# Performance work log

Measured on AMD Instinct MI355X. Metric: run time of the kernel, lower is better.

The kernel has to match this reference:

```python
import jax, jax.numpy as jnp
import numpy as np

B, T, N, H = 128, 512, 256, 1024  # batch, seq_len(input_size), num_nodes(params.input_size), hidden_size


def _glorot(k, shape):
    fan_in, fan_out = shape
    s = float(np.sqrt(6.0 / (fan_in + fan_out)))
    return jax.random.uniform(k, shape, minval=-s, maxval=s, dtype=jnp.float32)


def setup_inputs() -> dict:
    key = jax.random.key(0)
    ks = jax.random.split(key, 10)
    return {
        "x": jax.random.normal(ks[0], (B, T, N), dtype=jnp.float32),
        # SAGEConv 1: lin_l (neighbor mean, with bias), lin_r (root, no bias)
        "Wl1": _glorot(ks[1], (T, H)), "Wr1": _glorot(ks[2], (T, H)), "b1": jnp.zeros((H,), jnp.float32),
        # SAGEConv 2
        "Wl2": _glorot(ks[3], (H, H)), "Wr2": _glorot(ks[4], (H, H)), "b2": jnp.zeros((H,), jnp.float32),
        # block_1: Linear(H,H,bias=False), Linear(H,T,bias=False), Sigmoid
        "W1a": _glorot(ks[5], (H, H)), "W1b": _glorot(ks[6], (H, T)),
        # block_2: Linear(N,N,bias=False), Linear(N,H,bias=False), Sigmoid
        "W2a": _glorot(ks[7], (N, N)), "W2b": _glorot(ks[8], (N, H)),
    }


def _sage(h, Wl, Wr, b):
    # Dense graph without self-loops: mean over neighbors = (sum_all - self) / (n-1).
    n = h.shape[1]
    mean_nb = (jnp.sum(h, axis=1, keepdims=True) - h) / (n - 1)  # [B,N,F]
    return mean_nb @ Wl + h @ Wr + b  # SAGEConv: lin_l(aggr) + lin_r(x)


def reference(x, Wl1, Wr1, b1, Wl2, Wr2, b2, W1a, W1b, W2a, W2b):
    h = jnp.transpose(x, (0, 2, 1))            # [B,N,T] nodes=features
    h = _sage(h, Wl1, Wr1, b1)                 # [B,N,H]
    h = _sage(h, Wl2, Wr2, b2)                 # [B,N,H]
    h = jax.nn.sigmoid((h @ W1a) @ W1b)        # [B,N,T]
    h = jnp.transpose(h, (0, 2, 1))            # [B,T,N]
    return jax.nn.sigmoid((h @ W2a) @ W2b)     # [B,T,H]
```

## Files before the change

kernel.cpp:

```cpp
#include <hip/hip_runtime.h>
#include <hip/hip_bf16.h>

#define B_ 128
#define T_ 512
#define N_ 256
#define H_ 1024

typedef unsigned short u16;
typedef __attribute__((ext_vector_type(8))) __bf16 bf16x8;
typedef __attribute__((ext_vector_type(4))) float f32x4;

__device__ __forceinline__ u16 f2bf(float f) {
    unsigned u = __float_as_uint(f);
    u = (u + 0x7FFFu + ((u >> 16) & 1u)) >> 16;
    return (u16)u;
}

__device__ __forceinline__ void g2l16(const void* g, void* l) {
    __builtin_amdgcn_global_load_lds(
        (const __attribute__((address_space(1))) void*)g,
        (__attribute__((address_space(3))) void*)l,
        16, 0, 0);
}

#define ASLOT 12288u

#define GATE(N) { asm volatile("s_waitcnt vmcnt(" #N ")" ::: "memory"); \
                  __builtin_amdgcn_s_barrier(); }
#define LD4(dst, base) { _Pragma("unroll") for (int i_ = 0; i_ < 4; ++i_) \
    dst[i_] = *(const bf16x8*)(L + (base) + i_ * 512); }
#define STAGE(tile) { const u16* a_ = gA + (size_t)(tile) * 32; \
    const u16* b_ = gB + (size_t)(tile) * 32; \
    const unsigned s_ = (unsigned)(((tile) % 3) * ASLOT); \
    g2l16(a_, dA0 + s_);  g2l16(a_ + jstr, dA0 + s_ + 4096); \
    g2l16(b_, dB0 + s_); }
#define BODY(t) { \
    const unsigned sl = (unsigned)(((t) % 3) * ASLOT); \
    bf16x8 ra[4], rb[4]; \
    LD4(ra, sl + aoff); \
    LD4(rb, sl + boff); \
    if ((t) + 2 < nt) STAGE((t) + 2); \
    __builtin_amdgcn_s_setprio(1); \
    _Pragma("unroll") for (int mi_ = 0; mi_ < 4; ++mi_) \
    _Pragma("unroll") for (int ni_ = 0; ni_ < 4; ++ni_) \
        acc[mi_][ni_] = __builtin_amdgcn_mfma_f32_16x16x32_bf16( \
            ra[mi_], rb[ni_], acc[mi_][ni_], 0, 0, 0); \
    __builtin_amdgcn_s_setprio(0); }

template<int ACT, int OUT>
__global__ __launch_bounds__(512, 2) void gemm_e3(
    const u16* __restrict__ A, const u16* __restrict__ Bt,
    float* __restrict__ Cf, u16* __restrict__ Cb,
    const float* __restrict__ bias,
    int Nc, int K, int bshift, int gysh)
{
    __shared__ u16 L[36864];
    const int tid = threadIdx.x;
    const int wave = tid >> 6, lane = tid & 63;
    const int l16 = lane & 15, lh = lane >> 4;
    const int wm = wave >> 1, wn = wave & 1;

    const int qq = (int)gridDim.x >> 3;
    const int orig = (int)blockIdx.x;
    const int wg = (orig & 7) * qq + (orig >> 3);
    const int by = wg & ((1 << gysh) - 1), bx = wg >> gysh;
    const size_t m0 = (size_t)bx * 256, n0 = (size_t)by * 128;

    const int sx8 = (lh ^ ((l16 >> 1) & 3)) * 8;
    const unsigned aoff = (unsigned)(wm * 2048 + l16 * 32 + sx8);
    const unsigned boff = (unsigned)(8192 + wn * 2048 + l16 * 32 + sx8);

    const int srow = tid >> 2;
    const int sslot = (tid & 3) ^ ((srow >> 1) & 3);
    const size_t jstr = (size_t)128 * K;
    const u16* gA = A + (m0 + srow) * (size_t)K + sslot * 8;
    const u16* gB = Bt + (n0 + srow) * (size_t)K + sslot * 8;
    u16* const dA0 = L + (unsigned)(wave * 512);
    u16* const dB0 = L + 8192 + (unsigned)(wave * 512);

    f32x4 acc[4][4] = {};
    const int nt = K >> 5;

    STAGE(0); STAGE(1);
    for (int t = 0; t < nt - 1; ++t) {
        GATE(3);
        BODY(t);
    }
    GATE(0);
    { const int t = nt - 1; BODY(t); }

    const size_t NcS = (size_t)Nc;
    if (OUT == 2) {
        __syncthreads();
        const int P = 260;
#pragma unroll
        for (int mi = 0; mi < 4; ++mi) {
#pragma unroll
            for (int ni = 0; ni < 4; ++ni) {
                int tt = wn * 64 + ni * 16 + l16;
                int nn = wm * 64 + mi * 16 + lh * 4;
                u16 e[4];
#pragma unroll
                for (int rr = 0; rr < 4; ++rr) {
                    float v = acc[mi][ni][rr];
                    v = 1.0f / (1.0f + __expf(-v));
                    e[rr] = f2bf(v);
                }
                *(uint2*)&L[tt * P + nn] = *(const uint2*)e;
            }
        }
        __syncthreads();
        const int t = tid >> 2, seg = tid & 3;
        const u16* src = &L[t * P + seg * 64];
        uint2 u2[16];
#pragma unroll
        for (int j = 0; j < 16; ++j) u2[j] = *(const uint2*)&src[j * 4];
        const size_t b = m0 >> 8;
        u16* dst = Cb + ((b * T_ + (n0 + (size_t)t)) * N_ + seg * 64);
#pragma unroll
        for (int i = 0; i < 8; ++i) {
            uint4 w = make_uint4(u2[2 * i].x, u2[2 * i].y, u2[2 * i + 1].x, u2[2 * i + 1].y);
            ((uint4*)dst)[i] = w;
        }
    } else {
#pragma unroll
        for (int mi = 0; mi < 4; ++mi) {
#pragma unroll
            for (int ni = 0; ni < 4; ++ni) {
                size_t rbase = m0 + wm * 64 + mi * 16 + lh * 4;
                size_t col   = n0 + wn * 64 + ni * 16 + l16;
#pragma unroll
                for (int rr = 0; rr < 4; ++rr) {
                    size_t row = rbase + rr;
                    float v = acc[mi][ni][rr];
                    if (bias) v += bias[(row >> bshift) * NcS + col];
                    if (ACT) v = 1.0f / (1.0f + __expf(-v));
                    if (OUT == 1) __builtin_nontemporal_store(v, &Cf[row * NcS + col]);
                    else          Cb[row * NcS + col] = f2bf(v);
                }
            }
        }
    }
}

__device__ __forceinline__ void small_body(
    const u16* __restrict__ A, const u16* __restrict__ Bt,
    float* __restrict__ Cf, u16* __restrict__ Cb,
    const float* __restrict__ bias,
    int Nc, int K, int lda, int ldb, int outmode, int bshift,
    float kscale, float bmul, int bx, int by)
{
    __shared__ u16 lA[128 * 64];
    __shared__ u16 lB[128 * 64];
    const int tid = threadIdx.x;
    const int wave = tid >> 6, lane = tid & 63;
    const int l16 = lane & 15, lh = lane >> 4;
    const int wm = wave >> 1, wn = wave & 1;
    const long m0 = (long)bx * 128;
    const long n0 = (long)by * 128;

    f32x4 acc[4][4] = {};

    for (int k0 = 0; k0 < K; k0 += 64) {
#pragma unroll
        for (int j = 0; j < 4; ++j) {
            int c = j * 256 + tid;
            int row = c >> 3, col = (c & 7) << 3;
            g2l16(A  + (m0 + row) * (size_t)lda + k0 + col, &lA[(size_t)(j * 256 + (wave << 6)) * 8]);
            g2l16(Bt + (n0 + row) * (size_t)ldb + k0 + col, &lB[(size_t)(j * 256 + (wave << 6)) * 8]);
        }
        __syncthreads();
#pragma unroll
        for (int s = 0; s < 2; ++s) {
            bf16x8 af[4], bfr[4];
#pragma unroll
            for (int mi = 0; mi < 4; ++mi)
                af[mi] = *(const bf16x8*)&lA[((wm << 6) + (mi << 4) + l16) * 64 + s * 32 + (lh << 3)];
#pragma unroll
            for (int ni = 0; ni < 4; ++ni)
                bfr[ni] = *(const bf16x8*)&lB[((wn << 6) + (ni << 4) + l16) * 64 + s * 32 + (lh << 3)];
#pragma unroll
            for (int mi = 0; mi < 4; ++mi)
#pragma unroll
                for (int ni = 0; ni < 4; ++ni)
                    acc[mi][ni] = __builtin_amdgcn_mfma_f32_16x16x32_bf16(af[mi], bfr[ni], acc[mi][ni], 0, 0, 0);
        }
        __syncthreads();
    }

#pragma unroll
    for (int mi = 0; mi < 4; ++mi) {
#pragma unroll
        for (int ni = 0; ni < 4; ++ni) {
            long rbase = m0 + (wm << 6) + (mi << 4) + (lh << 2);
            long col   = n0 + (wn << 6) + (ni << 4) + l16;
#pragma unroll
            for (int r = 0; r < 4; ++r) {
                long row = rbase + r;
                float v = acc[mi][ni][r] * kscale;
                if (outmode == 2) {
                    v += (col < 1024 ? 1.0f : 256.0f / 255.0f) * bias[col & 1023];
                    Cb[(size_t)row * Nc + col] = f2bf(v);
                } else if (outmode == 3) {
                    if (bias) v += bmul * bias[(size_t)(row >> bshift) * Nc + col];
                    atomicAdd(&Cf[(size_t)row * Nc + col], v);
                } else {
                    if (bias) v += bmul * bias[(size_t)(row >> bshift) * Nc + col];
                    if (outmode == 1) Cf[(size_t)row * Nc + col] = v;
                    else              Cb[(size_t)row * Nc + col] = f2bf(v);
                }
            }
        }
    }
}

__global__ __launch_bounds__(256) void gemm_s23(
    const u16* __restrict__ Acat, const u16* __restrict__ W2cat,
    float* __restrict__ t12, const float* __restrict__ b2)
{
    small_body(Acat + blockIdx.x * 256, W2cat + blockIdx.x * 256, t12, nullptr,
               blockIdx.x == 0 ? b2 : nullptr,
               1024, 256, 2048, 2048, 3, 31, 1.0f, 1.0f, 0, blockIdx.y);
}

__global__ __launch_bounds__(256) void k_small4(
    const u16* __restrict__ W2cat, const u16* __restrict__ W1rm, u16* __restrict__ W12t,
    const u16* __restrict__ W1bt, const u16* __restrict__ W1ab, u16* __restrict__ W1ct,
    const u16* __restrict__ W2bt, const u16* __restrict__ W2ab, u16* __restrict__ W2ct,
    const u16* __restrict__ s1b, const u16* __restrict__ Wcat, u16* __restrict__ Acat,
    const float* __restrict__ b1)
{
    const int bid = blockIdx.x;
    if (bid < 32) {
        small_body(W2cat, W1rm, nullptr, W12t, nullptr, 512, 1024, 2048, 1024,
                   0, 0, 1.0f, 0.0f, bid >> 2, bid & 3);
    } else if (bid < 64) {
        int r = bid - 32;
        small_body(W1bt, W1ab, nullptr, W1ct, nullptr, 1024, 1024, 1024, 1024,
                   0, 0, 1.0f, 0.0f, r >> 3, r & 7);
    } else if (bid < 80) {
        int r = bid - 64;
        small_body(W2bt, W2ab, nullptr, W2ct, nullptr, 256, 256, 256, 256,
                   0, 0, 1.0f, 0.0f, r >> 1, r & 1);
    } else {
        int r = bid - 80;
        small_body(s1b, Wcat, nullptr, Acat, b1, 2048, 512, 512, 512,
                   2, 0, 1.0f / 255.0f, 0.0f, 0, r);
    }
}

__global__ __launch_bounds__(256) void k_prep(
    const float* __restrict__ Wl1, const float* __restrict__ Wr1,
    const float* __restrict__ Wl2, const float* __restrict__ Wr2,
    const float* __restrict__ W1b, const float* __restrict__ W2b,
    const float* __restrict__ W1a, const float* __restrict__ W2a,
    u16* __restrict__ Wcat, u16* __restrict__ W1rm,
    u16* __restrict__ W2cat,
    u16* __restrict__ W1bt, u16* __restrict__ W2bt,
    u16* __restrict__ W1ab, u16* __restrict__ W2ab,
    const float* __restrict__ x, u16* __restrict__ h, u16* __restrict__ s1b)
{
    __shared__ float smem[32 * 257];
    int bid = blockIdx.x;
    const int tx = threadIdx.x, ty = threadIdx.y;
    if (bid < 512) {
        float (*tl)[33] = (float(*)[33])smem;
        float (*tr)[33] = (float(*)[33])(smem + 32 * 33);
        int r0 = (bid >> 5) * 32, c0 = (bid & 31) * 32;
#pragma unroll
        for (int i = 0; i < 4; ++i) {
            int r = r0 + ty + 8 * i;
            float wl = Wl1[(size_t)r * H_ + c0 + tx];
            float wr = Wr1[(size_t)r * H_ + c0 + tx];
            tl[ty + 8 * i][tx] = wl;
            tr[ty + 8 * i][tx] = wl + wr;
            W1rm[(size_t)r * H_ + c0 + tx] = f2bf(wr - wl * (1.0f / 255.0f));
        }
        __syncthreads();
#pragma unroll
        for (int i = 0; i < 4; ++i) {
            size_t o = (size_t)(c0 + ty + 8 * i) * T_ + r0 + tx;
            Wcat[o]                     = f2bf(tl[tx][ty + 8 * i]);
            Wcat[o + (size_t)1024 * T_] = f2bf(tr[tx][ty + 8 * i]);
        }
    } else if (bid < 1536) {
        float (*tl)[33] = (float(*)[33])smem;
        float (*tr)[33] = (float(*)[33])(smem + 32 * 33);
        bid -= 512;
        int r0 = (bid >> 5) * 32, c0 = (bid & 31) * 32;
#pragma unroll
        for (int i = 0; i < 4; ++i) {
            int r = r0 + ty + 8 * i;
            float wl = Wl2[(size_t)r * H_ + c0 + tx];
            float wr = Wr2[(size_t)r * H_ + c0 + tx];
            tl[ty + 8 * i][tx] = wr - wl * (1.0f / 255.0f);
            tr[ty + 8 * i][tx] = wl;
        }
        __syncthreads();
#pragma unroll
        for (int i = 0; i < 4; ++i) {
            size_t o = (size_t)(c0 + ty + 8 * i) * 2048 + r0 + tx;
            W2cat[o]        = f2bf(tl[tx][ty + 8 * i]);
            W2cat[o + 1024] = f2bf(tr[tx][ty + 8 * i]);
        }
    } else if (bid < 2048) {
        float (*tl)[33] = (float(*)[33])smem;
        bid -= 1536;
        int r0 = (bid >> 4) * 32, c0 = (bid & 15) * 32;
#pragma unroll
        for (int i = 0; i < 4; ++i)
            tl[ty + 8 * i][tx] = W1b[(size_t)(r0 + ty + 8 * i) * T_ + c0 + tx];
        __syncthreads();
#pragma unroll
        for (int i = 0; i < 4; ++i)
            W1bt[(size_t)(c0 + ty + 8 * i) * H_ + r0 + tx] = f2bf(tl[tx][ty + 8 * i]);
    } else if (bid < 2304) {
        float (*tl)[33] = (float(*)[33])smem;
        bid -= 2048;
        int r0 = (bid >> 5) * 32, c0 = (bid & 31) * 32;
#pragma unroll
        for (int i = 0; i < 4; ++i)
            tl[ty + 8 * i][tx] = W2b[(size_t)(r0 + ty + 8 * i) * H_ + c0 + tx];
        __syncthreads();
#pragma unroll
        for (int i = 0; i < 4; ++i)
            W2bt[(size_t)(c0 + ty + 8 * i) * N_ + r0 + tx] = f2bf(tl[tx][ty + 8 * i]);
    } else if (bid < 2848) {
        int i = (bid - 2304) * 256 + ty * 32 + tx;
        const int n1 = H_ * H_ / 8;
        const float* s; u16* d;
        if (i < n1) { s = W1a; d = W1ab; }
        else        { s = W2a; d = W2ab; i -= n1; }
        float4 a = ((const float4*)s)[2 * i], b = ((const float4*)s)[2 * i + 1];
        u16 e[8] = {f2bf(a.x), f2bf(a.y), f2bf(a.z), f2bf(a.w),
                    f2bf(b.x), f2bf(b.y), f2bf(b.z), f2bf(b.w)};
        ((uint4*)d)[i] = *(const uint4*)e;
    } else {
        float (*sm)[257] = (float(*)[257])smem;
        int bid2 = bid - 2848;
        const int b = bid2 >> 4, t0 = (bid2 & 15) * 32;
        const int tid = ty * 32 + tx;
        const int wave = tid >> 6, lane = tid & 63;
        const float* xb = x + ((size_t)b * T_ + t0) * N_;
#pragma unroll
        for (int i = 0; i < 8; ++i) {
            int j = wave * 8 + i;
            float4 v = *(const float4*)(xb + (size_t)j * N_ + lane * 4);
            sm[j][lane * 4 + 0] = v.x;
            sm[j][lane * 4 + 1] = v.y;
            sm[j][lane * 4 + 2] = v.z;
            sm[j][lane * 4 + 3] = v.w;
        }
        __syncthreads();
#pragma unroll
        for (int i = 0; i < 8; ++i) {
            int j = wave * 8 + i;
            float s = sm[j][lane] + sm[j][lane + 64] + sm[j][lane + 128] + sm[j][lane + 192];
#pragma unroll
            for (int o = 32; o; o >>= 1) s += __shfl_down(s, o, 64);
            if (lane == 0) s1b[(size_t)b * T_ + t0 + j] = f2bf(s);
        }
        u16 e[32];
#pragma unroll
        for (int j = 0; j < 32; ++j) e[j] = f2bf(sm[j][tid]);
        uint4* dst = (uint4*)(h + ((size_t)b * N_ + tid) * T_ + t0);
        const uint4* src = (const uint4*)e;
#pragma unroll
        for (int v = 0; v < 4; ++v) dst[v] = src[v];
    }
}

extern "C" void kernel_launch(void* const* d_in, const int* in_sizes, int n_in,
                              void* d_out, int out_size, void* d_ws, size_t ws_size,
                              hipStream_t stream)
{
    const float* x   = (const float*)d_in[0];
    const float* Wl1 = (const float*)d_in[1];
    const float* Wr1 = (const float*)d_in[2];
    const float* b1  = (const float*)d_in[3];
    const float* Wl2 = (const float*)d_in[4];
    const float* Wr2 = (const float*)d_in[5];
    const float* b2  = (const float*)d_in[6];
    const float* W1a = (const float*)d_in[7];
    const float* W1b = (const float*)d_in[8];
    const float* W2a = (const float*)d_in[9];
    const float* W2b = (const float*)d_in[10];
    float* out = (float*)d_out;

    char* ws = (char*)d_ws;
    size_t off = 0;
    auto alloc = [&](size_t bytes) -> char* {
        char* p = ws + off;
        off += (bytes + 255) & ~(size_t)255;
        return p;
    };

    const size_t BN = (size_t)B_ * N_;
    const size_t BT = (size_t)B_ * T_;

    u16* h_bf   = (u16*)alloc(BN * T_ * 2);
    u16* h2_bf  = (u16*)alloc(BN * H_ * 2);
    u16* Wcat   = (u16*)alloc((size_t)2048 * T_ * 2);
    u16* W1rm   = (u16*)alloc((size_t)T_ * H_ * 2);
    u16* W2cat  = (u16*)alloc((size_t)H_ * 2048 * 2);
    u16* W1bt   = (u16*)alloc((size_t)T_ * H_ * 2);
    u16* W1ab   = (u16*)alloc((size_t)H_ * H_ * 2);
    u16* W1ct   = (u16*)alloc((size_t)T_ * H_ * 2);
    u16* W2bt   = (u16*)alloc((size_t)H_ * N_ * 2);
    u16* W2ab   = (u16*)alloc((size_t)N_ * N_ * 2);
    u16* W2ct   = (u16*)alloc((size_t)H_ * N_ * 2);
    u16* W12t   = (u16*)alloc((size_t)H_ * T_ * 2);
    u16* s1b    = (u16*)alloc(BT * 2);
    u16* Acat   = (u16*)alloc((size_t)B_ * 2048 * 2);
    float* t12  = (float*)alloc((size_t)B_ * H_ * 4);

    u16* q_bf = h_bf;

    hipMemsetAsync(t12, 0, (size_t)B_ * H_ * 4, stream);
    k_prep<<<dim3(4896), dim3(32, 8), 0, stream>>>(Wl1, Wr1, Wl2, Wr2, W1b, W2b, W1a, W2a,
                                                   Wcat, W1rm, W2cat, W1bt, W2bt, W1ab, W2ab,
                                                   x, h_bf, s1b);
    k_small4<<<dim3(96), 256, 0, stream>>>(W2cat, W1rm, W12t, W1bt, W1ab, W1ct,
                                           W2bt, W2ab, W2ct, s1b, Wcat, Acat, b1);
    gemm_s23<<<dim3(8, 8), 256, 0, stream>>>(Acat, W2cat, t12, b2);

    gemm_e3<0, 0><<<dim3(1024), 512, 0, stream>>>(h_bf, W12t, nullptr, h2_bf, t12, H_, T_, 8, 3);
    gemm_e3<1, 2><<<dim3(512), 512, 0, stream>>>(h2_bf, W1ct, nullptr, q_bf, nullptr, T_, H_, 0, 2);
    gemm_e3<1, 1><<<dim3(2048), 512, 0, stream>>>(q_bf, W2ct, out, nullptr, nullptr, H_, N_, 0, 3);
}
```

Baseline: 271.0 us.

## Shrink GEMM tiles to 128x128 with 256-thread blocks and double buffering

Replaces the 256x128 tile, 512-thread, triple-buffered GEMM kernel with a 128x128 tile, 256-thread kernel using double-buffered LDS and a single wait per k-step. This cuts LDS use and raises the number of resident blocks and the grid size, aiming for better occupancy and load balance across CUs. In exchange each tile reuses less data, and the prefetch depth drops from two tiles to one, so more global load latency may be exposed. The transposed sigmoid epilogue is reworked to stage through LDS in two halves to fit the smaller buffer.

```diff
diff --git a/kernel.cpp b/kernel.cpp
--- a/kernel.cpp
+++ b/kernel.cpp
@@ -23,7 +23,7 @@
         16, 0, 0);
 }
 
-#define ASLOT 12288u
+#define ASLOT 8192u
 
 #define GATE(N) { asm volatile("s_waitcnt vmcnt(" #N ")" ::: "memory"); \
                   __builtin_amdgcn_s_barrier(); }
@@ -31,30 +31,18 @@
     dst[i_] = *(const bf16x8*)(L + (base) + i_ * 512); }
 #define STAGE(tile) { const u16* a_ = gA + (size_t)(tile) * 32; \
     const u16* b_ = gB + (size_t)(tile) * 32; \
-    const unsigned s_ = (unsigned)(((tile) % 3) * ASLOT); \
-    g2l16(a_, dA0 + s_);  g2l16(a_ + jstr, dA0 + s_ + 4096); \
-    g2l16(b_, dB0 + s_); }
-#define BODY(t) { \
-    const unsigned sl = (unsigned)(((t) % 3) * ASLOT); \
-    bf16x8 ra[4], rb[4]; \
-    LD4(ra, sl + aoff); \
-    LD4(rb, sl + boff); \
-    if ((t) + 2 < nt) STAGE((t) + 2); \
-    __builtin_amdgcn_s_setprio(1); \
-    _Pragma("unroll") for (int mi_ = 0; mi_ < 4; ++mi_) \
-    _Pragma("unroll") for (int ni_ = 0; ni_ < 4; ++ni_) \
-        acc[mi_][ni_] = __builtin_amdgcn_mfma_f32_16x16x32_bf16( \
-            ra[mi_], rb[ni_], acc[mi_][ni_], 0, 0, 0); \
-    __builtin_amdgcn_s_setprio(0); }
+    const unsigned s_ = (unsigned)(((tile) & 1) * ASLOT); \
+    g2l16(a_, dA0 + s_);  g2l16(a_ + rstr, dA0 + s_ + 2048); \
+    g2l16(b_, dB0 + s_);  g2l16(b_ + rstr, dB0 + s_ + 2048); }
 
 template<int ACT, int OUT>
-__global__ __launch_bounds__(512, 2) void gemm_e3(
+__global__ __launch_bounds__(256, 4) void gemm_e4(
     const u16* __restrict__ A, const u16* __restrict__ Bt,
     float* __restrict__ Cf, u16* __restrict__ Cb,
     const float* __restrict__ bias,
     int Nc, int K, int bshift, int gysh)
 {
-    __shared__ u16 L[36864];
+    __shared__ u16 L[16384];
     const int tid = threadIdx.x;
     const int wave = tid >> 6, lane = tid & 63;
     const int l16 = lane & 15, lh = lane >> 4;
@@ -64,63 +52,75 @@
     const int orig = (int)blockIdx.x;
     const int wg = (orig & 7) * qq + (orig >> 3);
     const int by = wg & ((1 << gysh) - 1), bx = wg >> gysh;
-    const size_t m0 = (size_t)bx * 256, n0 = (size_t)by * 128;
+    const size_t m0 = (size_t)bx * 128, n0 = (size_t)by * 128;
 
     const int sx8 = (lh ^ ((l16 >> 1) & 3)) * 8;
     const unsigned aoff = (unsigned)(wm * 2048 + l16 * 32 + sx8);
-    const unsigned boff = (unsigned)(8192 + wn * 2048 + l16 * 32 + sx8);
+    const unsigned boff = (unsigned)(4096 + wn * 2048 + l16 * 32 + sx8);
 
     const int srow = tid >> 2;
     const int sslot = (tid & 3) ^ ((srow >> 1) & 3);
-    const size_t jstr = (size_t)128 * K;
+    const size_t rstr = (size_t)64 * K;
     const u16* gA = A + (m0 + srow) * (size_t)K + sslot * 8;
     const u16* gB = Bt + (n0 + srow) * (size_t)K + sslot * 8;
     u16* const dA0 = L + (unsigned)(wave * 512);
-    u16* const dB0 = L + 8192 + (unsigned)(wave * 512);
+    u16* const dB0 = L + 4096 + (unsigned)(wave * 512);
 
     f32x4 acc[4][4] = {};
     const int nt = K >> 5;
 
-    STAGE(0); STAGE(1);
-    for (int t = 0; t < nt - 1; ++t) {
-        GATE(3);
-        BODY(t);
-    }
-    GATE(0);
-    { const int t = nt - 1; BODY(t); }
+    STAGE(0);
+    for (int t = 0; t < nt; ++t) {
+        GATE(0);
+        const unsigned sl = (unsigned)((t & 1) * ASLOT);
+        bf16x8 ra[4], rb[4];
+        LD4(ra, sl + aoff);
+        LD4(rb, sl + boff);
+        if (t + 1 < nt) STAGE(t + 1);
+        __builtin_amdgcn_s_setprio(1);
+#pragma unroll
+        for (int mi = 0; mi < 4; ++mi)
+#pragma unroll
+            for (int ni = 0; ni < 4; ++ni)
+                acc[mi][ni] = __builtin_amdgcn_mfma_f32_16x16x32_bf16(
+                    ra[mi], rb[ni], acc[mi][ni], 0, 0, 0);
+        __builtin_amdgcn_s_setprio(0);
+    }
 
     const size_t NcS = (size_t)Nc;
     if (OUT == 2) {
-        __syncthreads();
-        const int P = 260;
-#pragma unroll
-        for (int mi = 0; mi < 4; ++mi) {
-#pragma unroll
-            for (int ni = 0; ni < 4; ++ni) {
-                int tt = wn * 64 + ni * 16 + l16;
-                int nn = wm * 64 + mi * 16 + lh * 4;
-                u16 e[4];
-#pragma unroll
-                for (int rr = 0; rr < 4; ++rr) {
-                    float v = acc[mi][ni][rr];
-                    v = 1.0f / (1.0f + __expf(-v));
-                    e[rr] = f2bf(v);
+        const int P = 132;
+        const size_t b = m0 >> 8;
+        const int nb = (int)(m0 & 255);
+        __syncthreads();
+#pragma unroll
+        for (int p = 0; p < 2; ++p) {
+            if (wn == p) {
+#pragma unroll
+                for (int mi = 0; mi < 4; ++mi) {
+#pragma unroll
+                    for (int ni = 0; ni < 4; ++ni) {
+                        int tt = ni * 16 + l16;
+                        int nn = wm * 64 + mi * 16 + lh * 4;
+                        u16 e[4];
+#pragma unroll
+                        for (int rr = 0; rr < 4; ++rr) {
+                            float v = acc[mi][ni][rr];
+                            v = 1.0f / (1.0f + __expf(-v));
+                            e[rr] = f2bf(v);
+                        }
+                        *(uint2*)&L[tt * P + nn] = *(const uint2*)e;
+                    }
                 }
-                *(uint2*)&L[tt * P + nn] = *(const uint2*)e;
             }
-        }
-        __syncthreads();
-        const int t = tid >> 2, seg = tid & 3;
-        const u16* src = &L[t * P + seg * 64];
-        uint2 u2[16];
-#pragma unroll
-        for (int j = 0; j < 16; ++j) u2[j] = *(const uint2*)&src[j * 4];
-        const size_t b = m0 >> 8;
-        u16* dst = Cb + ((b * T_ + (n0 + (size_t)t)) * N_ + seg * 64);
-#pragma unroll
-        for (int i = 0; i < 8; ++i) {
-            uint4 w = make_uint4(u2[2 * i].x, u2[2 * i].y, u2[2 * i + 1].x, u2[2 * i + 1].y);
-            ((uint4*)dst)[i] = w;
+            __syncthreads();
+            const int tp = tid >> 2, seg = tid & 3;
+            const u16* src = &L[tp * P + seg * 32];
+            u16* dst = Cb + ((b * T_ + (n0 + p * 64 + (size_t)tp)) * N_ + nb + seg * 32);
+#pragma unroll
+            for (int i = 0; i < 4; ++i)
+                ((uint4*)dst)[i] = *(const uint4*)&src[i * 8];
+            __syncthreads();
         }
     } else {
 #pragma unroll
@@ -424,7 +424,7 @@
                                            W2bt, W2ab, W2ct, s1b, Wcat, Acat, b1);
     gemm_s23<<<dim3(8, 8), 256, 0, stream>>>(Acat, W2cat, t12, b2);
 
-    gemm_e3<0, 0><<<dim3(1024), 512, 0, stream>>>(h_bf, W12t, nullptr, h2_bf, t12, H_, T_, 8, 3);
-    gemm_e3<1, 2><<<dim3(512), 512, 0, stream>>>(h2_bf, W1ct, nullptr, q_bf, nullptr, T_, H_, 0, 2);
-    gemm_e3<1, 1><<<dim3(2048), 512, 0, stream>>>(q_bf, W2ct, out, nullptr, nullptr, H_, N_, 0, 3);
-}
+    gemm_e4<0, 0><<<dim3(2048), 256, 0, stream>>>(h_bf, W12t, nullptr, h2_bf, t12, H_, T_, 8, 3);
+    gemm_e4<1, 2><<<dim3(1024), 256, 0, stream>>>(h2_bf, W1ct, nullptr, q_bf, nullptr, T_, H_, 0, 2);
+    gemm_e4<1, 1><<<dim3(4096), 256, 0, stream>>>(q_bf, W2ct, out, nullptr, nullptr, H_, N_, 0, 3);
+}
```

After: 294.9 us. +8.8%, slower.
